# Kernel optimization log

Hardware: AMD Instinct MI355X
Metric: run time of the kernel (lower is better)

The kernel has to match this reference:

```python
import jax, jax.numpy as jnp
from jax import lax
import numpy as np

Z, Y, X = 41, 256, 256  # sparse_shape = grid_size[::-1]
N_VOX = 60000
C_IN = 4
DN = ('NCDHW', 'OIDHW', 'NCDHW')


def _conv(x, w, stride=(1, 1, 1), pad=1):
    return lax.conv_general_dilated(x, w, stride, [(pad, pad)] * 3, dimension_numbers=DN)


def _tconv(x, w, stride=(2, 2, 2), pad=1, outpad=(0, 0, 0)):
    # torch ConvTranspose3d (weight [Cin,Cout,k,k,k]) == conv with lhs dilation,
    # spatially-flipped, in/out-swapped kernel, padding (k-1-p, k-1-p+output_padding)
    wt = jnp.flip(jnp.swapaxes(w, 0, 1), axis=(2, 3, 4))
    padding = [(2 - pad, 2 - pad + op) for op in outpad]  # k=3
    return lax.conv_general_dilated(x, wt, (1, 1, 1), padding, lhs_dilation=stride, dimension_numbers=DN)


def _bn_relu(y, s, b, m):
    # eval-mode BN folded into per-channel scale/shift, then ReLU, then restrict
    # to the sparse active-site mask (spconv only stores features at active sites)
    return jax.nn.relu(y * s[None, :, None, None, None] + b[None, :, None, None, None]) * m


def _forward(feats, params, coords, batch_size):
    (w1, s1, b1, w2a, s2a, b2a, w2b, s2b, b2b, w3a, s3a, b3a, w3b, s3b, b3b,
     w4a, s4a, b4a, w4b, s4b, b4b, w5a, s5a, b5a, w5b, s5b, b5b) = params
    B = batch_size
    bi, zi, yi, xi = coords[:, 0], coords[:, 1], coords[:, 2], coords[:, 3]
    dense = jnp.zeros((B, C_IN, Z, Y, X), feats.dtype).at[bi, :, zi, yi, xi].set(feats)
    m0 = jnp.zeros((B, 1, Z, Y, X), feats.dtype).at[bi, 0, zi, yi, xi].set(1.0)
    one = jnp.ones((1, 1, 3, 3, 3), feats.dtype)
    # conv1: SparseConv3d k3 s1 p1 -> active set dilates
    m1 = (_conv(m0, one) > 0).astype(feats.dtype)
    x = _bn_relu(_conv(dense, w1), s1, b1, m1)
    # conv2: SparseConv3d s2 + SubMConv3d (mask unchanged for subm)
    m2 = (_conv(m1, one, (2, 2, 2)) > 0).astype(feats.dtype)
    x = _bn_relu(_conv(x, w2a, (2, 2, 2)), s2a, b2a, m2)
    x = _bn_relu(_conv(x, w2b), s2b, b2b, m2)
    # conv3
    m3 = (_conv(m2, one, (2, 2, 2)) > 0).astype(feats.dtype)
    x = _bn_relu(_conv(x, w3a, (2, 2, 2)), s3a, b3a, m3)
    x = _bn_relu(_conv(x, w3b), s3b, b3b, m3)
    # deconv4: SparseConvTranspose3d s2 + subm
    m4 = (_tconv(m3, one) > 0).astype(feats.dtype)
    x = _bn_relu(_tconv(x, w4a), s4a, b4a, m4)
    x = _bn_relu(_conv(x, w4b), s4b, b4b, m4)
    # deconv5: output_padding (0,3,3) restores full Y/X resolution
    m5 = (_tconv(m4, one, outpad=(0, 3, 3)) > 0).astype(feats.dtype)
    x = _bn_relu(_tconv(x, w5a, outpad=(0, 3, 3)), s5a, b5a, m5)
    x = _bn_relu(_conv(x, w5b), s5b, b5b, m5)
    return x  # dense [B, 32, Z, Y, X]; zeros at inactive sites


def setup_inputs() -> dict:
    rng = np.random.default_rng(0)
    flat = rng.choice(Z * Y * X, size=N_VOX, replace=False)
    zi = (flat // (Y * X)).astype(np.int32)
    rem = flat % (Y * X)
    yi = (rem // X).astype(np.int32)
    xi = (rem % X).astype(np.int32)
    coords = np.stack([np.zeros(N_VOX, np.int32), zi, yi, xi], axis=1)

    def w(o, i):
        return jnp.asarray((rng.standard_normal((o, i, 3, 3, 3)) * 0.05).astype(np.float32))

    def scale(c):
        return jnp.asarray(rng.uniform(0.5, 1.5, c).astype(np.float32))

    def shift(c):
        return jnp.asarray((rng.standard_normal(c) * 0.1).astype(np.float32))

    return {
        'occ_voxel_features': jnp.asarray(rng.standard_normal((N_VOX, C_IN)).astype(np.float32)),
        'occ_voxel_coords': jnp.asarray(coords),
        'batch_size': 1,
        'w1': w(16, 4), 's1': scale(16), 'b1': shift(16),
        'w2a': w(32, 16), 's2a': scale(32), 'b2a': shift(32),
        'w2b': w(32, 32), 's2b': scale(32), 'b2b': shift(32),
        'w3a': w(64, 32), 's3a': scale(64), 'b3a': shift(64),
        'w3b': w(64, 64), 's3b': scale(64), 'b3b': shift(64),
        'w4a': w(64, 32), 's4a': scale(32), 'b4a': shift(32),  # transpose weight [Cin,Cout,...]
        'w4b': w(32, 32), 's4b': scale(32), 'b4b': shift(32),
        'w5a': w(32, 32), 's5a': scale(32), 'b5a': shift(32),
        'w5b': w(32, 32), 's5b': scale(32), 'b5b': shift(32),
    }


def reference(occ_voxel_features, occ_voxel_coords, batch_size,
              w1, s1, b1, w2a, s2a, b2a, w2b, s2b, b2b,
              w3a, s3a, b3a, w3b, s3b, b3b,
              w4a, s4a, b4a, w4b, s4b, b4b,
              w5a, s5a, b5a, w5b, s5b, b5b):
    params = (w1, s1, b1, w2a, s2a, b2a, w2b, s2b, b2b, w3a, s3a, b3a, w3b, s3b, b3b,
              w4a, s4a, b4a, w4b, s4b, b4b, w5a, s5a, b5a, w5b, s5b, b5b)
    return _forward(occ_voxel_features, params, occ_voxel_coords, batch_size)
```

## Files before the change

kernel.cpp:

```cpp
#include <hip/hip_runtime.h>
#include <hip/hip_bf16.h>
#include <stdint.h>

namespace {

constexpr int Z0 = 41, Y0 = 256, X0 = 256;
constexpr int Z2 = 21, Y2 = 128, X2 = 128;
constexpr int Z3 = 11, Y3 = 64,  X3 = 64;
constexpr int Z4 = 21, Y4 = 127, X4 = 127;
constexpr int NV0 = Z0 * Y0 * X0;
constexpr int NV2 = Z2 * Y2 * X2;
constexpr int NV3 = Z3 * Y3 * X3;
constexpr int NV4 = Z4 * Y4 * X4;

constexpr int ZP0 = 43, YP0 = 258, XP0 = 258; constexpr int NP0 = ZP0 * YP0 * XP0;
constexpr int ZP2 = 23, YP2 = 130, XP2 = 130; constexpr int NP2 = ZP2 * YP2 * XP2;
constexpr int ZP3 = 13, YP3 = 66,  XP3 = 66;  constexpr int NP3 = ZP3 * YP3 * XP3;
constexpr int ZP4 = 23, YP4 = 129, XP4 = 129; constexpr int NP4 = ZP4 * YP4 * XP4;

using bf16 = __hip_bfloat16;
typedef __attribute__((ext_vector_type(8))) short s16x8;
typedef __attribute__((ext_vector_type(4))) float f32x4;

__device__ inline unsigned f2b(float f) {
    return (unsigned)__builtin_bit_cast(unsigned short, __float2bfloat16(f));
}

__device__ inline int xcd_swz(int bid, int nwg) {
    int q = nwg >> 3, r = nwg & 7;
    int x = bid & 7, j = bid >> 3;
    return (x < r ? x * (q + 1) : r * (q + 1) + (x - r) * q) + j;
}

__device__ inline void glds16(const bf16* g, void* l) {
    __builtin_amdgcn_global_load_lds(
        (const __attribute__((address_space(1))) void*)g,
        (__attribute__((address_space(3))) void*)l, 16, 0, 0);
}

__global__ __launch_bounds__(256) void sentinel_k(float* out) { out[0] = 12345.0f; }

__global__ __launch_bounds__(256) void scatter_k(const float* __restrict__ feats,
                                                 const int* __restrict__ coords,
                                                 bf16* __restrict__ dense,
                                                 uint8_t* __restrict__ m0, int n) {
    int v = blockIdx.x * 256 + threadIdx.x;
    if (v >= n) return;
    int z = coords[v * 4 + 1], y = coords[v * 4 + 2], x = coords[v * 4 + 3];
    m0[(z * Y0 + y) * X0 + x] = 1;
    int pp = ((z + 1) * YP0 + (y + 1)) * XP0 + (x + 1);
    uint2 u;
    u.x = f2b(feats[v * 4 + 0]) | (f2b(feats[v * 4 + 1]) << 16);
    u.y = f2b(feats[v * 4 + 2]) | (f2b(feats[v * 4 + 3]) << 16);
    *(uint2*)(dense + (size_t)pp * 4) = u;
}

template <int C>
__global__ __launch_bounds__(256) void halo_zero_k(bf16* __restrict__ buf,
                                                   int Zi, int Yi, int Xi,
                                                   int Zp, int Yp, int Xp) {
    int i = blockIdx.x * 256 + threadIdx.x;
    int tot = Zp * Yp * Xp;
    if (i >= tot) return;
    int x = i % Xp; int t = i / Xp; int y = t % Yp; int z = t / Yp;
    bool halo = (z < 1) | (z > Zi) | (y < 1) | (y > Yi) | (x < 1) | (x > Xi);
    if (!halo) return;
    uint4 zz = make_uint4(0, 0, 0, 0);
    uint4* p = (uint4*)(buf + (size_t)i * C);
#pragma unroll
    for (int j = 0; j < C / 8; ++j) p[j] = zz;
}

__global__ __launch_bounds__(256) void repack_frag_k(const float* __restrict__ w,
                                                     bf16* __restrict__ wf,
                                                     int CIN, int COUT, int TRANS) {
    int NT = COUT / 16, KT = CIN / 32;
    int i = blockIdx.x * 256 + threadIdx.x;
    int total = 27 * NT * KT * 64;
    if (i >= total) return;
    int lane = i & 63; int t = i >> 6;
    int kt = t % KT; t /= KT; int nt = t % NT; int tap = t / NT;
    int co = nt * 16 + (lane & 15);
    int ci0 = kt * 32 + (lane >> 4) * 8;
    unsigned e[8];
#pragma unroll
    for (int j = 0; j < 8; ++j) {
        int ci = ci0 + j;
        int src = TRANS ? ((ci * COUT + co) * 27 + tap) : ((co * CIN + ci) * 27 + tap);
        e[j] = f2b(w[src]);
    }
    uint4 u;
    u.x = e[0] | (e[1] << 16); u.y = e[2] | (e[3] << 16);
    u.z = e[4] | (e[5] << 16); u.w = e[6] | (e[7] << 16);
    ((uint4*)wf)[i] = u;
}

__global__ __launch_bounds__(256) void repack_frag_c16_k(const float* __restrict__ w,
                                                         bf16* __restrict__ wf) {
    int i = blockIdx.x * 256 + threadIdx.x;
    int total = 14 * 2 * 64;
    if (i >= total) return;
    int lane = i & 63; int t = i >> 6;
    int nt = t & 1; int p = t >> 1;
    int lg = lane >> 4, lr = lane & 15;
    int co = nt * 16 + lr;
    unsigned e[8];
#pragma unroll
    for (int j = 0; j < 8; ++j) {
        int tap = 2 * p + (lg >> 1);
        int ci = (lg & 1) * 8 + j;
        e[j] = (tap < 27) ? f2b(w[(co * 16 + ci) * 27 + tap]) : 0u;
    }
    uint4 u;
    u.x = e[0] | (e[1] << 16); u.y = e[2] | (e[3] << 16);
    u.z = e[4] | (e[5] << 16); u.w = e[6] | (e[7] << 16);
    ((uint4*)wf)[i] = u;
}

__global__ __launch_bounds__(256) void repack_frag_l1_k(const float* __restrict__ w,
                                                        bf16* __restrict__ wf) {
    int i = blockIdx.x * 256 + threadIdx.x;
    if (i >= 256) return;
    int lane = i & 63, kb = i >> 6;
    int lg = lane >> 4, lr = lane & 15;
    unsigned e[8];
#pragma unroll
    for (int j = 0; j < 8; ++j) {
        int tap = kb * 8 + lg * 2 + (j >> 2);
        int ci = j & 3;
        e[j] = (tap < 27) ? f2b(w[(lr * 4 + ci) * 27 + tap]) : 0u;
    }
    uint4 u;
    u.x = e[0] | (e[1] << 16); u.y = e[2] | (e[3] << 16);
    u.z = e[4] | (e[5] << 16); u.w = e[6] | (e[7] << 16);
    ((uint4*)wf)[i] = u;
}

__global__ __launch_bounds__(256) void dilate_k(const uint8_t* __restrict__ in,
                                                uint8_t* __restrict__ out,
                                                int Zi, int Yi, int Xi,
                                                int Zo, int Yo, int Xo, int stride) {
    int idx = blockIdx.x * 256 + threadIdx.x;
    int total = Zo * Yo * Xo;
    if (idx >= total) return;
    int x = idx % Xo; int t = idx / Xo; int y = t % Yo; int z = t / Yo;
    int YX = Yi * Xi;
    uint8_t r = 0;
    for (int kz = 0; kz < 3; ++kz) {
        int zi = z * stride + kz - 1;
        if ((unsigned)zi >= (unsigned)Zi) continue;
        for (int ky = 0; ky < 3; ++ky) {
            int yi = y * stride + ky - 1;
            if ((unsigned)yi >= (unsigned)Yi) continue;
            for (int kx = 0; kx < 3; ++kx) {
                int xi = x * stride + kx - 1;
                if ((unsigned)xi >= (unsigned)Xi) continue;
                r |= in[zi * YX + yi * Xi + xi];
            }
        }
    }
    out[idx] = r ? 1 : 0;
}

__global__ __launch_bounds__(256) void dilate4_k(const uint8_t* __restrict__ in,
                                                 uint8_t* __restrict__ out,
                                                 int Z, int Y, int X) {
    int ngx = X >> 2;
    int g = blockIdx.x * 256 + threadIdx.x;
    int total = Z * Y * ngx;
    if (g >= total) return;
    int gx = g % ngx; int t = g / ngx; int y = t % Y; int z = t / Y;
    const int YX = Y * X;
    unsigned r = 0;
    for (int kz = 0; kz < 3; ++kz) {
        int zi = z + kz - 1;
        if ((unsigned)zi >= (unsigned)Z) continue;
        for (int ky = 0; ky < 3; ++ky) {
            int yi = y + ky - 1;
            if ((unsigned)yi >= (unsigned)Y) continue;
            const unsigned* rw = (const unsigned*)(in + zi * YX + yi * X);
            unsigned u1 = rw[gx];
            unsigned u0 = gx ? rw[gx - 1] : 0u;
            unsigned u2 = (gx + 1 < ngx) ? rw[gx + 1] : 0u;
            r |= u1 | ((u1 << 8) | (u0 >> 24)) | ((u1 >> 8) | (u2 << 24));
        }
    }
    r |= r >> 4; r |= r >> 2; r |= r >> 1; r &= 0x01010101u;
    ((unsigned*)out)[g] = r;
}

__global__ __launch_bounds__(256) void tdilate_k(const uint8_t* __restrict__ in,
                                                 uint8_t* __restrict__ out,
                                                 int Zi, int Yi, int Xi,
                                                 int Zo, int Yo, int Xo) {
    int idx = blockIdx.x * 256 + threadIdx.x;
    int total = Zo * Yo * Xo;
    if (idx >= total) return;
    int x = idx % Xo; int t = idx / Xo; int y = t % Yo; int z = t / Yo;
    int YX = Yi * Xi;
    uint8_t r = 0;
    for (int kz = 0; kz < 3; ++kz) {
        int tz = z + 1 - kz;
        if (tz & 1) continue;
        int zi = tz >> 1;
        if ((unsigned)zi >= (unsigned)Zi) continue;
        for (int ky = 0; ky < 3; ++ky) {
            int ty = y + 1 - ky;
            if (ty & 1) continue;
            int yi = ty >> 1;
            if ((unsigned)yi >= (unsigned)Yi) continue;
            for (int kx = 0; kx < 3; ++kx) {
                int tx = x + 1 - kx;
                if (tx & 1) continue;
                int xi = tx >> 1;
                if ((unsigned)xi >= (unsigned)Xi) continue;
                r |= in[zi * YX + yi * Xi + xi];
            }
        }
    }
    out[idx] = r ? 1 : 0;
}

__global__ __launch_bounds__(256) void tdilate4_k(const uint8_t* __restrict__ in,
                                                  uint8_t* __restrict__ out,
                                                  int Zi, int Yi, int Xi,
                                                  int Zo, int Yo, int Xo) {
    int ngx = Xo >> 2;
    int g = blockIdx.x * 256 + threadIdx.x;
    int total = Zo * Yo * ngx;
    if (g >= total) return;
    int gx = g % ngx; int t = g / ngx; int y = t % Yo; int z = t / Yo;
    int YX = Yi * Xi;
    int j0 = gx * 2;
    unsigned r0 = 0, r1 = 0, r2 = 0, r3 = 0;
    for (int kz = 0; kz < 3; ++kz) {
        int tz = z + 1 - kz;
        if (tz & 1) continue;
        int zi = tz >> 1;
        if ((unsigned)zi >= (unsigned)Zi) continue;
        for (int ky = 0; ky < 3; ++ky) {
            int ty = y + 1 - ky;
            if (ty & 1) continue;
            int yi = ty >> 1;
            if ((unsigned)yi >= (unsigned)Yi) continue;
            const uint8_t* rp = in + zi * YX + yi * Xi;
            unsigned b0 = (j0 < Xi) ? rp[j0] : 0u;
            unsigned b1 = (j0 + 1 < Xi) ? rp[j0 + 1] : 0u;
            unsigned b2 = (j0 + 2 < Xi) ? rp[j0 + 2] : 0u;
            r0 |= b0; r1 |= b0 | b1; r2 |= b1; r3 |= b1 | b2;
        }
    }
    unsigned rr = (r0 ? 1u : 0u) | (r1 ? 0x100u : 0u) | (r2 ? 0x10000u : 0u) | (r3 ? 0x1000000u : 0u);
    ((unsigned*)out)[g] = rr;
}

__global__ __launch_bounds__(256, 2) void conv_roll_k(
    const bf16* __restrict__ in, const bf16* __restrict__ wfrag,
    const float* __restrict__ scale, const float* __restrict__ shift,
    const uint8_t* __restrict__ mask, float* __restrict__ outf,
    int Zo, int Yo, int Xo, int Ypi, int Xpi, int nx) {
    constexpr int ROWB = 34 * 64;
    constexpr int SLABB = 4 * ROWB;
    __shared__ uint4 ring4[5 * SLABB / 16];
    char* ring = (char*)ring4;

    const int No = Zo * Yo * Xo;
    const int bid = xcd_swz(blockIdx.x, gridDim.x);
    const int tx = bid % nx, ty = bid / nx;
    const int y0 = ty * 2, x0 = tx * 32;

    const int tid = threadIdx.x;
    const int w = tid >> 6, lane = tid & 63;
    const int lg = lane >> 4, lr = lane & 15;
    const int yr = w >> 1, ch = w & 1;

    auto stagefn = [&](int zp, int slot) {
        int zs = zp <= Zo + 1 ? zp : Zo + 1;
        char* slab = ring + slot * SLABB + w * ROWB;
        const bf16* pb = in + ((size_t)zs * Ypi + (y0 + w)) * (size_t)Xpi * 32 + (size_t)x0 * 32;
        int u0 = lane;      glds16(pb + (u0 ^ ((u0 >> 3) & 7)) * 8, slab + u0 * 16);
        int u1 = 64 + lane; glds16(pb + (u1 ^ ((u1 >> 3) & 7)) * 8, slab + u1 * 16);
        if (lane < 8) { int u2 = 128 + lane; glds16(pb + u2 * 8, slab + u2 * 16); }
    };

    const uint4* gw = (const uint4*)wfrag;
    uint4 breg[27];
#pragma unroll
    for (int t = 0; t < 27; ++t) breg[t] = gw[(t * 2 + ch) * 64 + lane];

    int asw0[3], asw1[3];
#pragma unroll
    for (int dx = 0; dx < 3; ++dx) {
        int b0 = (lr + dx) * 64 + lg * 16;       asw0[dx] = b0 ^ (((b0 >> 7) & 7) << 4);
        int b1 = (16 + lr + dx) * 64 + lg * 16;  asw1[dx] = b1 ^ (((b1 >> 7) & 7) << 4);
    }

    const int co = ch * 16 + lr;
    const float sc = scale[co], sh = shift[co];

    stagefn(0, 0); stagefn(1, 1); stagefn(2, 2); stagefn(3, 3);
    uint mk0, mk1;
    {
        const uint8_t* mrow = mask + (size_t)(y0 + yr) * Xo + x0;
        mk0 = *(const uint*)(mrow + lg * 4);
        mk1 = *(const uint*)(mrow + 16 + lg * 4);
    }
    asm volatile("s_waitcnt vmcnt(0)" ::: "memory");
    __builtin_amdgcn_s_barrier();

    int rs0 = 0, wslot = 4;
    for (int z = 0; z < Zo; ++z) {
        uint nk0, nk1;
        {
            int zn = (z + 1 < Zo) ? z + 1 : Zo - 1;
            const uint8_t* mrow = mask + ((size_t)zn * Yo + (y0 + yr)) * Xo + x0;
            nk0 = *(const uint*)(mrow + lg * 4);
            nk1 = *(const uint*)(mrow + 16 + lg * 4);
        }
        stagefn(z + 4, wslot);

        int rs1 = rs0 + 1 < 5 ? rs0 + 1 : 0;
        int rs2 = rs1 + 1 < 5 ? rs1 + 1 : 0;
        const char* sl_0 = ring + rs0 * SLABB;
        const char* sl_1 = ring + rs1 * SLABB;
        const char* sl_2 = ring + rs2 * SLABB;

        f32x4 acc0 = (f32x4){0, 0, 0, 0}, acc1 = (f32x4){0, 0, 0, 0};
#pragma unroll
        for (int dz = 0; dz < 3; ++dz) {
            const char* slab = dz == 0 ? sl_0 : (dz == 1 ? sl_1 : sl_2);
#pragma unroll
            for (int dy = 0; dy < 3; ++dy) {
                const char* rowp = slab + (yr + dy) * ROWB;
#pragma unroll
                for (int dx = 0; dx < 3; ++dx) {
                    const int tap = dz * 9 + dy * 3 + dx;
                    uint4 a0 = *(const uint4*)(rowp + asw0[dx]);
                    uint4 a1 = *(const uint4*)(rowp + asw1[dx]);
                    acc0 = __builtin_amdgcn_mfma_f32_16x16x32_bf16(
                        __builtin_bit_cast(s16x8, a0), __builtin_bit_cast(s16x8, breg[tap]),
                        acc0, 0, 0, 0);
                    acc1 = __builtin_amdgcn_mfma_f32_16x16x32_bf16(
                        __builtin_bit_cast(s16x8, a1), __builtin_bit_cast(s16x8, breg[tap]),
                        acc1, 0, 0, 0);
                }
            }
        }

        const size_t rowbase = ((size_t)z * Yo + (y0 + yr)) * Xo + x0;
        {
            f32x4 o0, o1;
#pragma unroll
            for (int r = 0; r < 4; ++r) {
                float m0f = (float)((mk0 >> (8 * r)) & 1);
                float m1f = (float)((mk1 >> (8 * r)) & 1);
                o0[r] = fmaxf(fmaf(acc0[r], sc, sh), 0.f) * m0f;
                o1[r] = fmaxf(fmaf(acc1[r], sc, sh), 0.f) * m1f;
            }
            *(f32x4*)(outf + (size_t)co * No + rowbase + lg * 4)      = o0;
            *(f32x4*)(outf + (size_t)co * No + rowbase + 16 + lg * 4) = o1;
        }

        asm volatile("s_waitcnt vmcnt(9)" ::: "memory");
        __builtin_amdgcn_s_barrier();
        rs0 = rs1;
        wslot = wslot + 1 < 5 ? wslot + 1 : 0;
        mk0 = nk0; mk1 = nk1;
    }
}

__global__ __launch_bounds__(256, 3) void tconv_roll_k(
    const bf16* __restrict__ in, const bf16* __restrict__ wfrag,
    const float* __restrict__ scale, const float* __restrict__ shift,
    const uint8_t* __restrict__ mask, bf16* __restrict__ out,
    int Zo, int Yo, int Xo, int Zi, int Ypi, int Xpi, int Ypo, int Xpo, int nx) {
    constexpr int ROWB = 34 * 64;
    constexpr int SLABB = 3 * ROWB;
    __shared__ uint4 ring4[4 * SLABB / 16];
    char* ring = (char*)ring4;

    const int oct = blockIdx.y;
    const int pz = oct >> 2, py = (oct >> 1) & 1, px = oct & 1;
    const int Zq = (Zo - pz + 1) >> 1;

    const int bid = xcd_swz(blockIdx.x, gridDim.x);
    const int tx = bid % nx, ty = bid / nx;
    const int yq0 = ty * 2, xq0 = tx * 32;

    const int tid = threadIdx.x;
    const int w = tid >> 6, lane = tid & 63;
    const int lg = lane >> 4, lr = lane & 15;
    const int yr = w >> 1, xh = w & 1;

    const int kz0 = pz ? 0 : 1, dzo0 = pz ? 1 : 0;
    const int ky0 = py ? 0 : 1, dyo0 = py ? 1 : 0;
    const int kx0 = px ? 0 : 1, dxo0 = px ? 1 : 0;

    auto stagefn = [&](int p, int slot) {
        if (w < 3) {
            int zs = p < Zi ? p : Zi - 1;
            char* slab = ring + slot * SLABB + w * ROWB;
            const bf16* pb = in + ((size_t)(zs + 1) * Ypi + (yq0 + 1 + w)) * (size_t)Xpi * 32
                                + (size_t)(xq0 + 1) * 32;
            int u0 = lane;      glds16(pb + (u0 ^ ((u0 >> 3) & 7)) * 8, slab + u0 * 16);
            int u1 = 64 + lane; glds16(pb + (u1 ^ ((u1 >> 3) & 7)) * 8, slab + u1 * 16);
            if (lane < 8) { int u2 = 128 + lane; glds16(pb + u2 * 8, slab + u2 * 16); }
        }
    };

    const uint4* gw = (const uint4*)wfrag;
    uint4 breg[2][2][2][2];
#pragma unroll
    for (int iz = 0; iz < 2; ++iz) {
        int kz = iz ? 2 : kz0;
#pragma unroll
        for (int iy = 0; iy < 2; ++iy) {
            int ky = iy ? 2 : ky0;
#pragma unroll
            for (int ix = 0; ix < 2; ++ix) {
                int kx = ix ? 2 : kx0;
                int tap = kz * 9 + ky * 3 + kx;
                breg[iz][iy][ix][0] = gw[(tap * 2 + 0) * 64 + lane];
                breg[iz][iy][ix][1] = gw[(tap * 2 + 1) * 64 + lane];
            }
        }
    }

    int b0 = (xh * 16 + lr + dxo0) * 64 + lg * 16;
    int b1 = (xh * 16 + lr) * 64 + lg * 16;
    const int aswA = b0 ^ (((b0 >> 7) & 7) << 4);
    const int aswB = b1 ^ (((b1 >> 7) & 7) << 4);
    const int rowA = (yr + dyo0) * ROWB;
    const int rowB = yr * ROWB;

    const float sc0 = scale[lr], sh0 = shift[lr];
    const float sc1 = scale[16 + lr], sh1 = shift[16 + lr];

    const int yout = 2 * (yq0 + yr) + py;
    const int xb = 2 * (xq0 + xh * 16 + lg * 4) + px;

    stagefn(0, 0); stagefn(1, 1); stagefn(2, 2);
    uint2 mv;
    mv = *(const uint2*)(mask + ((size_t)pz * Yo + yout) * Xo + (xb - px));
    asm volatile("s_waitcnt vmcnt(0)" ::: "memory");
    __builtin_amdgcn_s_barrier();

    int rs0 = 0, wslot = 3;
    for (int zq = 0; zq < Zq; ++zq) {
        uint2 nv;
        {
            int zqn = (zq + 1 < Zq) ? zq + 1 : Zq - 1;
            nv = *(const uint2*)(mask + ((size_t)(2 * zqn + pz) * Yo + yout) * Xo + (xb - px));
        }
        stagefn(zq + 3, wslot);

        int rs1 = rs0 + 1 < 4 ? rs0 + 1 : 0;
        const char* sl_0 = ring + rs0 * SLABB;
        const char* sl_1 = ring + rs1 * SLABB;
        const char* slz0 = pz ? sl_1 : sl_0;
        const char* slz1 = sl_0;

        f32x4 acc0 = (f32x4){0, 0, 0, 0}, acc1 = (f32x4){0, 0, 0, 0};
#pragma unroll
        for (int iz = 0; iz < 2; ++iz) {
            if (iz > pz) continue;
            const char* slab = iz ? slz1 : slz0;
#pragma unroll
            for (int iy = 0; iy < 2; ++iy) {
                if (iy > py) continue;
                const char* rowp = slab + (iy ? rowB : rowA);
#pragma unroll
                for (int ix = 0; ix < 2; ++ix) {
                    if (ix > px) continue;
                    uint4 a = *(const uint4*)(rowp + (ix ? aswB : aswA));
                    acc0 = __builtin_amdgcn_mfma_f32_16x16x32_bf16(
                        __builtin_bit_cast(s16x8, a),
                        __builtin_bit_cast(s16x8, breg[iz][iy][ix][0]), acc0, 0, 0, 0);
                    acc1 = __builtin_amdgcn_mfma_f32_16x16x32_bf16(
                        __builtin_bit_cast(s16x8, a),
                        __builtin_bit_cast(s16x8, breg[iz][iy][ix][1]), acc1, 0, 0, 0);
                }
            }
        }

        const int zout = 2 * zq + pz;
        const size_t opdbase = ((size_t)(zout + 1) * Ypo + (yout + 1)) * Xpo;
#pragma unroll
        for (int r = 0; r < 4; ++r) {
            unsigned word = (r < 2) ? mv.x : mv.y;
            float m = (float)((word >> (px * 8 + (r & 1) * 16)) & 1);
            float v0 = fmaxf(fmaf(acc0[r], sc0, sh0), 0.f) * m;
            float v1 = fmaxf(fmaf(acc1[r], sc1, sh1), 0.f) * m;
            size_t opd = opdbase + (size_t)(xb + 2 * r + 1);
            out[opd * 32 + lr]      = __float2bfloat16(v0);
            out[opd * 32 + 16 + lr] = __float2bfloat16(v1);
        }

        asm volatile("s_waitcnt vmcnt(20)" ::: "memory");
        __builtin_amdgcn_s_barrier();
        rs0 = rs1;
        wslot = wslot + 1 < 4 ? wslot + 1 : 0;
        mv = nv;
    }
}

template <bool FINAL>
__global__ __launch_bounds__(512, 4) void conv_lds_k(
    const bf16* __restrict__ in, const bf16* __restrict__ wfrag,
    const float* __restrict__ scale, const float* __restrict__ shift,
    const uint8_t* __restrict__ mask, bf16* __restrict__ out, float* __restrict__ outf,
    int Zo, int Yo, int Xo, int Ypi, int Xpi, int Ypo, int Xpo, int nx, int ny) {
    constexpr int ROWB = 34 * 64;
    __shared__ uint4 tile4[36 * ROWB / 16];
    char* tile = (char*)tile4;

    const int No = Zo * Yo * Xo;
    const int bid = xcd_swz(blockIdx.x, gridDim.x);
    int tx = bid % nx; int tt = bid / nx; int ty = tt % ny; int tz = tt / ny;
    const int z0 = tz * 4, y0 = ty * 4, x0 = tx * 32;

    const int tid = threadIdx.x;
    const int w = tid >> 6, lane = tid & 63, lg = lane >> 4, lr = lane & 15;

    int anywork;
    {
        int row = tid >> 5, xl = tid & 31;
        int zz = z0 + (row >> 2), yy = y0 + (row & 3), xx = x0 + xl;
        int ok = (zz < Zo) && (yy < Yo) && (xx < Xo) && mask[((size_t)zz * Yo + yy) * Xo + xx];
        anywork = __syncthreads_or(ok);
    }

    f32x4 acc[4][2];
#pragma unroll
    for (int s = 0; s < 4; ++s) { acc[s][0] = (f32x4){0,0,0,0}; acc[s][1] = (f32x4){0,0,0,0}; }

    if (anywork) {
        const int lsw = (lane ^ ((lane >> 3) & 7)) * 8;
        for (int rr = w; rr < 36; rr += 8) {
            int dz = rr / 6, dy = rr % 6;
            const bf16* g = in + ((size_t)(z0 + dz) * Ypi + (y0 + dy)) * Xpi * 32 + (size_t)x0 * 32;
            char* l = tile + rr * ROWB;
            glds16(g + lsw, l);
            glds16(g + 512 + lsw, l + 1024);
            if (lane < 8) glds16(g + 1024 + lane * 8, l + 2048);
        }
        asm volatile("s_waitcnt vmcnt(0)" ::: "memory");
        __syncthreads();

        int rbB[4], bsw[4][3];
#pragma unroll
        for (int s = 0; s < 4; ++s) {
            int lrow = 2 * w + (s >> 1);
            rbB[s] = ((lrow >> 2) * 6 + (lrow & 3)) * ROWB;
            int xpart = (s & 1) * 16 + lr;
#pragma unroll
            for (int dx = 0; dx < 3; ++dx) {
                int b = (xpart + dx) * 64 + lg * 16;
                bsw[s][dx] = b ^ (((b >> 7) & 7) << 4);
            }
// ... 361 lines not shown
        }
#pragma unroll
        for (int nt = 0; nt < NT; ++nt) {
            int co = nt * 16 + lr;
            float sc = scale[co], sh = shift[co];
#pragma unroll
            for (int r = 0; r < 4; ++r) {
                if (!ok[r]) continue;
                float yv = fmaxf(fmaf(acc[s][nt][r], sc, sh), 0.f) * mm[r];
                out[(size_t)opd[r] * COUT + co] = __float2bfloat16(yv);
            }
        }
    }
}

__global__ __launch_bounds__(256, 4) void conv_l1_mfma_k(
    const bf16* __restrict__ in, const bf16* __restrict__ wfrag,
    const float* __restrict__ scale, const float* __restrict__ shift,
    const uint8_t* __restrict__ mask, bf16* __restrict__ out,
    int Zo, int Yo, int Xo, int Ypi, int Xpi, int Ypo, int Xpo) {
    const int No = Zo * Yo * Xo;
    const int bid = xcd_swz(blockIdx.x, gridDim.x);
    const int tid = threadIdx.x;
    const int wv = tid >> 6, lane = tid & 63;
    const int lg = lane >> 4, lr = lane & 15;
    const int v0 = bid * 256 + wv * 64;
    if (v0 >= No) return;

    int vm = v0 + lane;
    bool mw = (vm < No) && (mask[vm] != 0);
    const bool anywork = (__ballot(mw) != 0ull);

    f32x4 acc[4];
#pragma unroll
    for (int s = 0; s < 4; ++s) acc[s] = (f32x4){0.f, 0.f, 0.f, 0.f};

    if (anywork) {
        const uint4* gw = (const uint4*)wfrag;
        uint4 bu[4];
#pragma unroll
        for (int kb = 0; kb < 4; ++kb) bu[kb] = gw[kb * 64 + lane];

        int vtf[4][2];
#pragma unroll
        for (int kb = 0; kb < 4; ++kb)
#pragma unroll
            for (int u = 0; u < 2; ++u) {
                int tp = kb * 8 + lg * 2 + u;
                int kz = tp / 9, r9 = tp - kz * 9, ky = r9 / 3, kx = r9 - ky * 3;
                vtf[kb][u] = (tp < 27) ? (((kz - 1) * Ypi + (ky - 1)) * Xpi + (kx - 1)) : 0;
            }

        int pV[4];
#pragma unroll
        for (int s = 0; s < 4; ++s) {
            int vr = v0 + s * 16 + lr;
            if (vr >= No) vr = 0;
            int zz = vr / (Yo * Xo); int rr = vr - zz * (Yo * Xo);
            int yy = rr / Xo; int xx = rr - yy * Xo;
            pV[s] = ((zz + 1) * Ypi + (yy + 1)) * Xpi + (xx + 1);
        }

#pragma unroll
        for (int kb = 0; kb < 4; ++kb) {
#pragma unroll
            for (int s = 0; s < 4; ++s) {
                uint2 a0 = *(const uint2*)(in + (size_t)(pV[s] + vtf[kb][0]) * 4);
                uint2 a1 = *(const uint2*)(in + (size_t)(pV[s] + vtf[kb][1]) * 4);
                int4 ai; ai.x = a0.x; ai.y = a0.y; ai.z = a1.x; ai.w = a1.y;
                acc[s] = __builtin_amdgcn_mfma_f32_16x16x32_bf16(
                    __builtin_bit_cast(s16x8, ai),
                    __builtin_bit_cast(s16x8, bu[kb]), acc[s], 0, 0, 0);
            }
        }
    }

#pragma unroll
    for (int s = 0; s < 4; ++s) {
        const int vb = v0 + s * 16 + lg * 4;
        int co = lr;
        float sc = scale[co], sh = shift[co];
#pragma unroll
        for (int r = 0; r < 4; ++r) {
            int v = vb + r;
            if (v >= No) continue;
            float mm = mask[v] ? 1.f : 0.f;
            int zz = v / (Yo * Xo); int rr = v - zz * (Yo * Xo);
            int yy = rr / Xo; int xx = rr - yy * Xo;
            int opd = ((zz + 1) * Ypo + (yy + 1)) * Xpo + (xx + 1);
            float yv = fmaxf(fmaf(acc[s][r], sc, sh), 0.f) * mm;
            out[(size_t)opd * 16 + co] = __float2bfloat16(yv);
        }
    }
}

inline int nblk(int n) { return (n + 255) / 256; }
inline int cdiv(int a, int b) { return (a + b - 1) / b; }

}

extern "C" void kernel_launch(void* const* d_in, const int* in_sizes, int n_in,
                              void* d_out, int out_size, void* d_ws, size_t ws_size,
                              hipStream_t stream) {
    const float* feats = (const float*)d_in[0];
    const int* coords = (const int*)d_in[1];
    const int NVOX = in_sizes[0] / 4;

    const float *w1 = (const float*)d_in[3], *s1 = (const float*)d_in[4], *b1 = (const float*)d_in[5];
    const float *w2a = (const float*)d_in[6], *s2a = (const float*)d_in[7], *b2a = (const float*)d_in[8];
    const float *w2b = (const float*)d_in[9], *s2b = (const float*)d_in[10], *b2b = (const float*)d_in[11];
    const float *w3a = (const float*)d_in[12], *s3a = (const float*)d_in[13], *b3a = (const float*)d_in[14];
    const float *w3b = (const float*)d_in[15], *s3b = (const float*)d_in[16], *b3b = (const float*)d_in[17];
    const float *w4a = (const float*)d_in[18], *s4a = (const float*)d_in[19], *b4a = (const float*)d_in[20];
    const float *w4b = (const float*)d_in[21], *s4b = (const float*)d_in[22], *b4b = (const float*)d_in[23];
    const float *w5a = (const float*)d_in[24], *s5a = (const float*)d_in[25], *b5a = (const float*)d_in[26];
    const float *w5b = (const float*)d_in[27], *s5b = (const float*)d_in[28], *b5b = (const float*)d_in[29];

    char* ws = (char*)d_ws;
    size_t off = 0;
    auto alloc = [&](size_t bytes) -> void* {
        void* p = ws + off;
        off = (off + bytes + 255) & ~(size_t)255;
        return p;
    };

    uint8_t* m0 = (uint8_t*)alloc(NV0);
    uint8_t* m1 = (uint8_t*)alloc(NV0);
    uint8_t* m2 = (uint8_t*)alloc(NV2);
    uint8_t* m3 = (uint8_t*)alloc(NV3);
    uint8_t* m4 = (uint8_t*)alloc(NV4);
    uint8_t* m5 = (uint8_t*)alloc(NV0);

    bf16* slot0 = (bf16*)alloc((size_t)NP0 * 32 * 2);
    bf16* slot1 = (bf16*)alloc((size_t)NP0 * 16 * 2);

    bf16* dense0 = slot0;
    bf16* x1     = slot1;
    bf16* x2a    = slot0;
    bf16* x2b    = slot1;
    bf16* x3a    = slot0;
    bf16* x3b    = slot1;
    bf16* x4a    = slot0;
    bf16* x4b    = slot1;
    bf16* x5a    = slot0;

    bf16* wfL1 = (bf16*)alloc(4 * 64 * 8 * 2);
    bf16* wf2a = (bf16*)alloc((size_t)14 * 2 * 64 * 16);
    bf16* wf2b = (bf16*)alloc((size_t)27 * 2 * 1 * 64 * 16);
    bf16* wf3a = (bf16*)alloc((size_t)27 * 4 * 1 * 64 * 16);
    bf16* wf3b = (bf16*)alloc((size_t)27 * 4 * 2 * 64 * 16);
    bf16* wf4a = (bf16*)alloc((size_t)27 * 2 * 2 * 64 * 16);
    bf16* wf4b = (bf16*)alloc((size_t)27 * 2 * 1 * 64 * 16);
    bf16* wf5a = (bf16*)alloc((size_t)27 * 2 * 1 * 64 * 16);
    bf16* wf5b = (bf16*)alloc((size_t)27 * 2 * 1 * 64 * 16);
    alloc(20u << 20);

    if (off > ws_size) {
        sentinel_k<<<1, 256, 0, stream>>>((float*)d_out);
        return;
    }

    hipMemsetAsync(dense0, 0, (size_t)NP0 * 4 * 2, stream);
    hipMemsetAsync(m0, 0, NV0, stream);
    repack_frag_l1_k<<<1, 256, 0, stream>>>(w1, wfL1);
    repack_frag_c16_k<<<nblk(14 * 2 * 64), 256, 0, stream>>>(w2a, wf2a);
    repack_frag_k<<<nblk(27 * 2 * 64), 256, 0, stream>>>(w2b, wf2b, 32, 32, 0);
    repack_frag_k<<<nblk(27 * 4 * 64), 256, 0, stream>>>(w3a, wf3a, 32, 64, 0);
    repack_frag_k<<<nblk(27 * 8 * 64), 256, 0, stream>>>(w3b, wf3b, 64, 64, 0);
    repack_frag_k<<<nblk(27 * 4 * 64), 256, 0, stream>>>(w4a, wf4a, 64, 32, 1);
    repack_frag_k<<<nblk(27 * 2 * 64), 256, 0, stream>>>(w4b, wf4b, 32, 32, 0);
    repack_frag_k<<<nblk(27 * 2 * 64), 256, 0, stream>>>(w5a, wf5a, 32, 32, 1);
    repack_frag_k<<<nblk(27 * 2 * 64), 256, 0, stream>>>(w5b, wf5b, 32, 32, 0);

    scatter_k<<<nblk(NVOX), 256, 0, stream>>>(feats, coords, dense0, m0, NVOX);

    dilate4_k<<<nblk(NV0 / 4), 256, 0, stream>>>(m0, m1, Z0, Y0, X0);
    halo_zero_k<16><<<nblk(NP0), 256, 0, stream>>>(x1, Z0, Y0, X0, ZP0, YP0, XP0);
    conv_l1_mfma_k<<<nblk(NV0), 256, 0, stream>>>(
        dense0, wfL1, s1, b1, m1, x1, Z0, Y0, X0, YP0, XP0, YP0, XP0);

    dilate_k<<<nblk(NV2), 256, 0, stream>>>(m1, m2, Z0, Y0, X0, Z2, Y2, X2, 2);
    halo_zero_k<32><<<nblk(NP2), 256, 0, stream>>>(x2a, Z2, Y2, X2, ZP2, YP2, XP2);
    conv_s2c16_k<<<nblk(NV2), 256, 0, stream>>>(
        x1, wf2a, s2a, b2a, m2, x2a, Z2, Y2, X2, YP0, XP0, YP2, XP2);
    halo_zero_k<32><<<nblk(NP2), 256, 0, stream>>>(x2b, Z2, Y2, X2, ZP2, YP2, XP2);
    {
        int nx = cdiv(X2, 32), ny = cdiv(Y2, 4), nz = cdiv(Z2, 4);
        conv_lds_k<false><<<nx * ny * nz, 512, 0, stream>>>(
            x2a, wf2b, s2b, b2b, m2, x2b, nullptr, Z2, Y2, X2, YP2, XP2, YP2, XP2, nx, ny);
    }

    dilate_k<<<nblk(NV3), 256, 0, stream>>>(m2, m3, Z2, Y2, X2, Z3, Y3, X3, 2);
    halo_zero_k<64><<<nblk(NP3), 256, 0, stream>>>(x3a, Z3, Y3, X3, ZP3, YP3, XP3);
    conv_mfma_k<32, 64, 2, 64, false><<<cdiv(NV3, 64), 64, 0, stream>>>(
        x2b, wf3a, s3a, b3a, m3, x3a, nullptr, Z3, Y3, X3, YP2, XP2, YP3, XP3);
    halo_zero_k<64><<<nblk(NP3), 256, 0, stream>>>(x3b, Z3, Y3, X3, ZP3, YP3, XP3);
    conv_mfma_k<64, 64, 1, 64, false><<<cdiv(NV3, 64), 64, 0, stream>>>(
        x3a, wf3b, s3b, b3b, m3, x3b, nullptr, Z3, Y3, X3, YP3, XP3, YP3, XP3);

    tdilate_k<<<nblk(NV4), 256, 0, stream>>>(m3, m4, Z3, Y3, X3, Z4, Y4, X4);
    halo_zero_k<32><<<nblk(NP4), 256, 0, stream>>>(x4a, Z4, Y4, X4, ZP4, YP4, XP4);
    {
        int maxNq = ((Z4 + 1) >> 1) * ((Y4 + 1) >> 1) * ((X4 + 1) >> 1);
        dim3 g(nblk(maxNq), 8);
        tconv_mfma_k<64, 32><<<g, 256, 0, stream>>>(
            x3b, wf4a, s4a, b4a, m4, x4a, Z4, Y4, X4, YP3, XP3, YP4, XP4);
    }
    halo_zero_k<32><<<nblk(NP2), 256, 0, stream>>>(x4b, Z4, Y4, X4, ZP2, YP2, XP2);
    {
        int nx = cdiv(X4, 32), ny = cdiv(Y4, 4), nz = cdiv(Z4, 4);
        conv_lds_k<false><<<nx * ny * nz, 512, 0, stream>>>(
            x4a, wf4b, s4b, b4b, m4, x4b, nullptr, Z4, Y4, X4, YP4, XP4, YP2, XP2, nx, ny);
    }

    tdilate4_k<<<nblk(NV0 / 4), 256, 0, stream>>>(m4, m5, Z4, Y4, X4, Z0, Y0, X0);
    halo_zero_k<32><<<nblk(NP0), 256, 0, stream>>>(x5a, Z0, Y0, X0, ZP0, YP0, XP0);
    {
        dim3 g((Y0 / 2 / 2) * (X0 / 2 / 32), 8);
        tconv_roll_k<<<g, 256, 0, stream>>>(
            x4b, wf5a, s5a, b5a, m5, x5a, Z0, Y0, X0, Z4, YP2, XP2, YP0, XP0, X0 / 2 / 32);
    }
    {
        int nx = X0 / 32, ny = Y0 / 2;
        conv_roll_k<<<nx * ny, 256, 0, stream>>>(
            x5a, wf5b, s5b, b5b, m5, (float*)d_out, Z0, Y0, X0, YP0, XP0, nx);
    }
}
```

Baseline: 866.1 us.

## Retile final submanifold conv onto 32x32x16 MFMA with 8-row blocks

The last full-resolution conv is rewritten so each 512-thread block covers 8 output rows by 32 columns. Each wave uses 32x32x16 bf16 MFMAs that produce all 32 output channels at once. A new weight repack kernel builds the 32-wide fragments, and the LDS ring is restaged to a new swizzled layout that shares the y-halo across more rows. The goal is to cut redundant halo loads and MFMA issue count, at the cost of a much larger LDS footprint per block, which limits occupancy. The tconv staging call also drops per-lane LDS offsets, which the hardware treats as wave-uniform anyway.

```diff
diff --git a/kernel.cpp b/kernel.cpp
--- a/kernel.cpp
+++ b/kernel.cpp
@@ -21,6 +21,8 @@
 using bf16 = __hip_bfloat16;
 typedef __attribute__((ext_vector_type(8))) short s16x8;
 typedef __attribute__((ext_vector_type(4))) float f32x4;
+typedef __attribute__((ext_vector_type(16))) float f32x16;
+typedef __attribute__((ext_vector_type(4))) unsigned u32x4;
 
 __device__ inline unsigned f2b(float f) {
     return (unsigned)__builtin_bit_cast(unsigned short, __float2bfloat16(f));
@@ -88,6 +90,25 @@
         int ci = ci0 + j;
         int src = TRANS ? ((ci * COUT + co) * 27 + tap) : ((co * CIN + ci) * 27 + tap);
         e[j] = f2b(w[src]);
+    }
+    uint4 u;
+    u.x = e[0] | (e[1] << 16); u.y = e[2] | (e[3] << 16);
+    u.z = e[4] | (e[5] << 16); u.w = e[6] | (e[7] << 16);
+    ((uint4*)wf)[i] = u;
+}
+
+__global__ __launch_bounds__(256) void repack_frag32_k(const float* __restrict__ w,
+                                                       bf16* __restrict__ wf) {
+    int i = blockIdx.x * 256 + threadIdx.x;
+    if (i >= 27 * 2 * 64) return;
+    int lane = i & 63; int t2 = i >> 6;
+    int ks = t2 & 1; int tap = t2 >> 1;
+    int co = lane & 31; int h = lane >> 5;
+    unsigned e[8];
+#pragma unroll
+    for (int j = 0; j < 8; ++j) {
+        int cin = ks * 16 + h * 8 + j;
+        e[j] = f2b(w[(co * 32 + cin) * 27 + tap]);
     }
     uint4 u;
     u.x = e[0] | (e[1] << 16); u.y = e[2] | (e[3] << 16);
@@ -254,118 +275,126 @@
     ((unsigned*)out)[g] = rr;
 }
 
-__global__ __launch_bounds__(256, 2) void conv_roll_k(
+__global__ __launch_bounds__(512, 2) void conv_roll_k(
     const bf16* __restrict__ in, const bf16* __restrict__ wfrag,
     const float* __restrict__ scale, const float* __restrict__ shift,
-    const uint8_t* __restrict__ mask, float* __restrict__ outf,
-    int Zo, int Yo, int Xo, int Ypi, int Xpi, int nx) {
-    constexpr int ROWB = 34 * 64;
-    constexpr int SLABB = 4 * ROWB;
+    const uint8_t* __restrict__ mask, float* __restrict__ outf) {
+    constexpr int ROWB = 2176;
+    constexpr int SLABB = 24576;
     __shared__ uint4 ring4[5 * SLABB / 16];
     char* ring = (char*)ring4;
 
-    const int No = Zo * Yo * Xo;
     const int bid = xcd_swz(blockIdx.x, gridDim.x);
-    const int tx = bid % nx, ty = bid / nx;
-    const int y0 = ty * 2, x0 = tx * 32;
+    const int tx = bid & 7, ty = bid >> 3;
+    const int y0 = ty * 8, x0 = tx * 32;
 
     const int tid = threadIdx.x;
     const int w = tid >> 6, lane = tid & 63;
-    const int lg = lane >> 4, lr = lane & 15;
-    const int yr = w >> 1, ch = w & 1;
-
-    auto stagefn = [&](int zp, int slot) {
-        int zs = zp <= Zo + 1 ? zp : Zo + 1;
-        char* slab = ring + slot * SLABB + w * ROWB;
-        const bf16* pb = in + ((size_t)zs * Ypi + (y0 + w)) * (size_t)Xpi * 32 + (size_t)x0 * 32;
-        int u0 = lane;      glds16(pb + (u0 ^ ((u0 >> 3) & 7)) * 8, slab + u0 * 16);
-        int u1 = 64 + lane; glds16(pb + (u1 ^ ((u1 >> 3) & 7)) * 8, slab + u1 * 16);
-        if (lane < 8) { int u2 = 128 + lane; glds16(pb + u2 * 8, slab + u2 * 16); }
+    const int vx = lane & 31, h = lane >> 5;
+    const int yr = w;
+
+    int soff[3];
+#pragma unroll
+    for (int k = 0; k < 3; ++k) {
+        int i = tid + k * 512;
+        int ii = i < 1360 ? i : 0;
+        int row = ii / 136, L = ii - row * 136;
+        int ks = L / 68, r2 = L - ks * 68, v = r2 >> 1, hh = r2 & 1;
+        int vs = v ^ ((v >> 2) & 3);
+        soff[k] = ((y0 + row) * XP0 + (x0 + vs)) * 32 + (2 * ks + hh) * 8;
+    }
+    auto stagefn = [&](int p, char* slab) {
+        int zs = p < ZP0 ? p : ZP0 - 1;
+        const bf16* pb = in + (size_t)zs * ((size_t)YP0 * XP0 * 32);
+        glds16(pb + soff[0], slab + w * 1024);
+        glds16(pb + soff[1], slab + w * 1024 + 8192);
+        glds16(pb + soff[2], slab + w * 1024 + 16384);
     };
 
-    const uint4* gw = (const uint4*)wfrag;
-    uint4 breg[27];
-#pragma unroll
-    for (int t = 0; t < 27; ++t) breg[t] = gw[(t * 2 + ch) * 64 + lane];
-
-    int asw0[3], asw1[3];
+    const u32x4* gw = (const u32x4*)wfrag;
+    u32x4 breg[27][2];
+#pragma unroll
+    for (int t = 0; t < 27; ++t) {
+        breg[t][0] = gw[(t * 2 + 0) * 64 + lane];
+        breg[t][1] = gw[(t * 2 + 1) * 64 + lane];
+    }
+#pragma unroll
+    for (int t = 0; t < 27; ++t)
+        asm volatile("" : "+v"(breg[t][0]), "+v"(breg[t][1]));
+
+    int asw[3];
 #pragma unroll
     for (int dx = 0; dx < 3; ++dx) {
-        int b0 = (lr + dx) * 64 + lg * 16;       asw0[dx] = b0 ^ (((b0 >> 7) & 7) << 4);
-        int b1 = (16 + lr + dx) * 64 + lg * 16;  asw1[dx] = b1 ^ (((b1 >> 7) & 7) << 4);
-    }
-
-    const int co = ch * 16 + lr;
-    const float sc = scale[co], sh = shift[co];
-
-    stagefn(0, 0); stagefn(1, 1); stagefn(2, 2); stagefn(3, 3);
-    uint mk0, mk1;
-    {
-        const uint8_t* mrow = mask + (size_t)(y0 + yr) * Xo + x0;
-        mk0 = *(const uint*)(mrow + lg * 4);
-        mk1 = *(const uint*)(mrow + 16 + lg * 4);
-    }
+        int v = vx + dx;
+        asw[dx] = (v ^ ((v >> 2) & 3)) * 32 + h * 16;
+    }
+
+    const float sc = scale[vx], sh = shift[vx];
+
+    stagefn(0, ring);
+    stagefn(1, ring + SLABB);
+    stagefn(2, ring + 2 * SLABB);
+    stagefn(3, ring + 3 * SLABB);
+    stagefn(4, ring + 4 * SLABB);
     asm volatile("s_waitcnt vmcnt(0)" ::: "memory");
     __builtin_amdgcn_s_barrier();
 
-    int rs0 = 0, wslot = 4;
-    for (int z = 0; z < Zo; ++z) {
-        uint nk0, nk1;
-        {
-            int zn = (z + 1 < Zo) ? z + 1 : Zo - 1;
-            const uint8_t* mrow = mask + ((size_t)zn * Yo + (y0 + yr)) * Xo + x0;
-            nk0 = *(const uint*)(mrow + lg * 4);
-            nk1 = *(const uint*)(mrow + 16 + lg * 4);
-        }
-        stagefn(z + 4, wslot);
-
-        int rs1 = rs0 + 1 < 5 ? rs0 + 1 : 0;
-        int rs2 = rs1 + 1 < 5 ? rs1 + 1 : 0;
-        const char* sl_0 = ring + rs0 * SLABB;
-        const char* sl_1 = ring + rs1 * SLABB;
-        const char* sl_2 = ring + rs2 * SLABB;
-
-        f32x4 acc0 = (f32x4){0, 0, 0, 0}, acc1 = (f32x4){0, 0, 0, 0};
+    int s0 = 0;
+    for (int z = 0; z < Z0; ++z) {
+        const int s1 = s0 + 1 < 5 ? s0 + 1 : 0;
+        const int s2 = s1 + 1 < 5 ? s1 + 1 : 0;
+        const char* sl0 = ring + s0 * SLABB;
+        const char* sl1 = ring + s1 * SLABB;
+        const char* sl2 = ring + s2 * SLABB;
+
+        f32x16 acc;
+#pragma unroll
+        for (int i = 0; i < 16; ++i) acc[i] = 0.f;
+
 #pragma unroll
         for (int dz = 0; dz < 3; ++dz) {
-            const char* slab = dz == 0 ? sl_0 : (dz == 1 ? sl_1 : sl_2);
+            const char* slab = dz == 0 ? sl0 : (dz == 1 ? sl1 : sl2);
 #pragma unroll
             for (int dy = 0; dy < 3; ++dy) {
                 const char* rowp = slab + (yr + dy) * ROWB;
 #pragma unroll
                 for (int dx = 0; dx < 3; ++dx) {
                     const int tap = dz * 9 + dy * 3 + dx;
-                    uint4 a0 = *(const uint4*)(rowp + asw0[dx]);
-                    uint4 a1 = *(const uint4*)(rowp + asw1[dx]);
-                    acc0 = __builtin_amdgcn_mfma_f32_16x16x32_bf16(
-                        __builtin_bit_cast(s16x8, a0), __builtin_bit_cast(s16x8, breg[tap]),
-                        acc0, 0, 0, 0);
-                    acc1 = __builtin_amdgcn_mfma_f32_16x16x32_bf16(
-                        __builtin_bit_cast(s16x8, a1), __builtin_bit_cast(s16x8, breg[tap]),
-                        acc1, 0, 0, 0);
+                    u32x4 a0 = *(const u32x4*)(rowp + asw[dx]);
+                    u32x4 a1 = *(const u32x4*)(rowp + 1088 + asw[dx]);
+                    acc = __builtin_amdgcn_mfma_f32_32x32x16_bf16(
+                        __builtin_bit_cast(s16x8, a0),
+                        __builtin_bit_cast(s16x8, breg[tap][0]), acc, 0, 0, 0);
+                    acc = __builtin_amdgcn_mfma_f32_32x32x16_bf16(
+                        __builtin_bit_cast(s16x8, a1),
+                        __builtin_bit_cast(s16x8, breg[tap][1]), acc, 0, 0, 0);
                 }
             }
         }
 
-        const size_t rowbase = ((size_t)z * Yo + (y0 + yr)) * Xo + x0;
-        {
-            f32x4 o0, o1;
+        const uint8_t* mrow = mask + ((size_t)z * Y0 + (y0 + yr)) * X0 + x0 + 4 * h;
+        unsigned mq0 = *(const unsigned*)(mrow);
+        unsigned mq1 = *(const unsigned*)(mrow + 8);
+        unsigned mq2 = *(const unsigned*)(mrow + 16);
+        unsigned mq3 = *(const unsigned*)(mrow + 24);
+
+        const size_t obase = (size_t)vx * NV0 + ((size_t)z * Y0 + (y0 + yr)) * X0 + x0 + 4 * h;
+#pragma unroll
+        for (int q = 0; q < 4; ++q) {
+            unsigned mq = q == 0 ? mq0 : (q == 1 ? mq1 : (q == 2 ? mq2 : mq3));
+            f32x4 o;
 #pragma unroll
             for (int r = 0; r < 4; ++r) {
-                float m0f = (float)((mk0 >> (8 * r)) & 1);
-                float m1f = (float)((mk1 >> (8 * r)) & 1);
-                o0[r] = fmaxf(fmaf(acc0[r], sc, sh), 0.f) * m0f;
-                o1[r] = fmaxf(fmaf(acc1[r], sc, sh), 0.f) * m1f;
-            }
-            *(f32x4*)(outf + (size_t)co * No + rowbase + lg * 4)      = o0;
-            *(f32x4*)(outf + (size_t)co * No + rowbase + 16 + lg * 4) = o1;
-        }
-
-        asm volatile("s_waitcnt vmcnt(9)" ::: "memory");
+                float m = (float)((mq >> (8 * r)) & 1);
+                o[r] = fmaxf(fmaf(acc[q * 4 + r], sc, sh), 0.f) * m;
+            }
+            *(f32x4*)(outf + obase + 8 * q) = o;
+        }
+
         __builtin_amdgcn_s_barrier();
-        rs0 = rs1;
-        wslot = wslot + 1 < 5 ? wslot + 1 : 0;
-        mk0 = nk0; mk1 = nk1;
+        stagefn(z + 5, ring + s0 * SLABB);
+        asm volatile("s_waitcnt vmcnt(11)" ::: "memory");
+        s0 = s1;
     }
 }
 
@@ -402,9 +431,9 @@
             char* slab = ring + slot * SLABB + w * ROWB;
             const bf16* pb = in + ((size_t)(zs + 1) * Ypi + (yq0 + 1 + w)) * (size_t)Xpi * 32
                                 + (size_t)(xq0 + 1) * 32;
-            int u0 = lane;      glds16(pb + (u0 ^ ((u0 >> 3) & 7)) * 8, slab + u0 * 16);
-            int u1 = 64 + lane; glds16(pb + (u1 ^ ((u1 >> 3) & 7)) * 8, slab + u1 * 16);
-            if (lane < 8) { int u2 = 128 + lane; glds16(pb + u2 * 8, slab + u2 * 16); }
+            int u0 = lane;      glds16(pb + (u0 ^ ((u0 >> 3) & 7)) * 8, slab);
+            int u1 = 64 + lane; glds16(pb + (u1 ^ ((u1 >> 3) & 7)) * 8, slab + 1024);
+            if (lane < 8) { int u2 = 128 + lane; glds16(pb + u2 * 8, slab + 2048); }
         }
     };
 
@@ -1072,7 +1101,7 @@
     bf16* wf4a = (bf16*)alloc((size_t)27 * 2 * 2 * 64 * 16);
     bf16* wf4b = (bf16*)alloc((size_t)27 * 2 * 1 * 64 * 16);
     bf16* wf5a = (bf16*)alloc((size_t)27 * 2 * 1 * 64 * 16);
-    bf16* wf5b = (bf16*)alloc((size_t)27 * 2 * 1 * 64 * 16);
+    bf16* wf5b32 = (bf16*)alloc((size_t)27 * 2 * 64 * 16);
     alloc(20u << 20);
 
     if (off > ws_size) {
@@ -1090,7 +1119,7 @@
     repack_frag_k<<<nblk(27 * 4 * 64), 256, 0, stream>>>(w4a, wf4a, 64, 32, 1);
     repack_frag_k<<<nblk(27 * 2 * 64), 256, 0, stream>>>(w4b, wf4b, 32, 32, 0);
     repack_frag_k<<<nblk(27 * 2 * 64), 256, 0, stream>>>(w5a, wf5a, 32, 32, 1);
-    repack_frag_k<<<nblk(27 * 2 * 64), 256, 0, stream>>>(w5b, wf5b, 32, 32, 0);
+    repack_frag32_k<<<nblk(27 * 2 * 64), 256, 0, stream>>>(w5b, wf5b32);
 
     scatter_k<<<nblk(NVOX), 256, 0, stream>>>(feats, coords, dense0, m0, NVOX);
 
@@ -1141,8 +1170,7 @@
             x4b, wf5a, s5a, b5a, m5, x5a, Z0, Y0, X0, Z4, YP2, XP2, YP0, XP0, X0 / 2 / 32);
     }
     {
-        int nx = X0 / 32, ny = Y0 / 2;
-        conv_roll_k<<<nx * ny, 256, 0, stream>>>(
-            x5a, wf5b, s5b, b5b, m5, (float*)d_out, Z0, Y0, X0, YP0, XP0, nx);
-    }
-}
+        conv_roll_k<<<(X0 / 32) * (Y0 / 8), 512, 0, stream>>>(
+            x5a, wf5b32, s5b, b5b, m5, (float*)d_out);
+    }
+}
```

After: 864.7 us. No clear change (-0.2%).
